# Performance work log

Measured on AMD Instinct MI355X. Metric: run time of the kernel, lower is better.

## Reference

```python
import jax, jax.numpy as jnp
import numpy as np

N, T, H, D, E, P, R = 50000, 16, 512, 256, 200000, 100000, 3
LN_EPS = 1e-5
BN_EPS = 1e-5


def setup_inputs() -> dict:
    key = jax.random.key(0)
    ks = jax.random.split(key, 32)
    ri = lambda k, shape, hi: jax.random.randint(k, shape, 0, hi)
    rn = lambda k, shape, scale=0.05: (jax.random.normal(k, shape, dtype=jnp.float32) * scale)
    return {
        "node_type_ids": ri(ks[0], (N,), T),
        "src0": ri(ks[1], (E,), N), "dst0": ri(ks[2], (E,), N),
        "src1": ri(ks[3], (E,), N), "dst1": ri(ks[4], (E,), N),
        "src2": ri(ks[5], (E,), N), "dst2": ri(ks[6], (E,), N),
        "pairs": ri(ks[7], (2, P), N),
        "degrees": ri(ks[8], (N,), 100),
        "node_emb": rn(ks[9], (N, H)),
        "type_emb": rn(ks[10], (T, H)),
        "w_loop_in": rn(ks[11], (H, H)),
        "w_rel_in": rn(ks[12], (R, H, H)),
        "w_loop_res": rn(ks[13], (H, H)),
        "w_rel_res": rn(ks[14], (R, H, H)),
        "ln_g": jnp.ones((H,), jnp.float32),
        "ln_b": jnp.zeros((H,), jnp.float32),
        "w_loop_out": rn(ks[15], (H, D)),
        "w_rel_out": rn(ks[16], (R, H, D)),
        "lp_w1": rn(ks[17], (3 * D, D)),
        "lp_b1": jnp.zeros((D,), jnp.float32),
        "bn_g": jnp.ones((D,), jnp.float32),
        "bn_b": jnp.zeros((D,), jnp.float32),
        "bn_mean": jnp.zeros((D,), jnp.float32),
        "bn_var": jnp.ones((D,), jnp.float32),
        "lp_w2": rn(ks[18], (D, 1)),
        "lp_b2": jnp.zeros((1,), jnp.float32),
        "alpha": jnp.float32(0.1),
        "beta": jnp.float32(0.1),
    }


def _rgcn(x, loop_w, rel_w, srcs, dsts):
    # out = x @ W_loop + sum_r (A_r @ x) @ W_r ; A_r unweighted COO -> segment_sum
    out = x @ loop_w
    for r in range(R):
        msg = jax.ops.segment_sum(x[srcs[r]], dsts[r], num_segments=x.shape[0])
        out = out + msg @ rel_w[r]
    return out


def _layernorm(h, g, b):
    mu = h.mean(-1, keepdims=True)
    var = h.var(-1, keepdims=True)
    return (h - mu) * jax.lax.rsqrt(var + LN_EPS) * g + b


def reference(node_type_ids, src0, dst0, src1, dst1, src2, dst2, pairs, degrees,
              node_emb, type_emb, w_loop_in, w_rel_in, w_loop_res, w_rel_res,
              ln_g, ln_b, w_loop_out, w_rel_out, lp_w1, lp_b1, bn_g, bn_b,
              bn_mean, bn_var, lp_w2, lp_b2, alpha, beta):
    srcs = (src0, src1, src2)
    dsts = (dst0, dst1, dst2)
    # encode
    x = node_emb + type_emb[node_type_ids]          # [N, H]
    x = jax.nn.relu(_rgcn(x, w_loop_in, w_rel_in, srcs, dsts))
    h = _rgcn(x, w_loop_res, w_rel_res, srcs, dsts)
    h = jax.nn.relu(_layernorm(h, ln_g, ln_b))      # dropout p=0 -> identity
    x = x + h
    z = _rgcn(x, w_loop_out, w_rel_out, srcs, dsts)  # [N, D]
    # score
    src_z = z[pairs[0]]                              # [P, D]
    dst_z = z[pairs[1]]
    src_deg = jnp.clip(degrees[pairs[0]], 1).astype(jnp.float32)
    dst_deg = jnp.clip(degrees[pairs[1]], 1).astype(jnp.float32)
    feats = jnp.concatenate([src_z, dst_z, src_z * dst_z], axis=-1)  # [P, 3D]
    h1 = jax.nn.relu(feats @ lp_w1 + lp_b1)
    # BatchNorm1d in eval mode: running stats
    h1 = (h1 - bn_mean) * jax.lax.rsqrt(bn_var + BN_EPS) * bn_g + bn_b
    mlp_score = (h1 @ lp_w2 + lp_b2).squeeze(-1)     # [P]
    base = mlp_score - jax.nn.relu(alpha) * jnp.log(src_deg) - jax.nn.relu(beta) * jnp.log(dst_deg)
    return base / (jnp.sqrt(src_deg) * jnp.sqrt(dst_deg) + 1e-8)
```

## Files before the change

### kernel.cpp

```cpp
#include <hip/hip_runtime.h>

typedef __attribute__((ext_vector_type(8))) _Float16 half8;
typedef __attribute__((ext_vector_type(4))) _Float16 half4;
typedef __attribute__((ext_vector_type(4))) float f32x4;

static __device__ __forceinline__ void gload16(const void* g, void* l) {
  __builtin_amdgcn_global_load_lds((const __attribute__((address_space(1))) void*)g,
                                   (__attribute__((address_space(3))) void*)l, 16, 0, 0);
}

__global__ void k_encode(const float* __restrict__ emb, const float* __restrict__ temb,
                         const int* __restrict__ tids, _Float16* __restrict__ x, int n) {
  int i = blockIdx.x * 256 + threadIdx.x;
  if (i >= n * 64) return;
  int node = i >> 6, c = (i & 63) << 3;
  const float* e = emb + (size_t)node * 512 + c;
  const float* t = temb + (size_t)tids[node] * 512 + c;
  float4 a0 = *(const float4*)e, a1 = *(const float4*)(e + 4);
  float4 b0 = *(const float4*)t, b1 = *(const float4*)(t + 4);
  half8 o;
  o[0] = (_Float16)(a0.x + b0.x); o[1] = (_Float16)(a0.y + b0.y);
  o[2] = (_Float16)(a0.z + b0.z); o[3] = (_Float16)(a0.w + b0.w);
  o[4] = (_Float16)(a1.x + b1.x); o[5] = (_Float16)(a1.y + b1.y);
  o[6] = (_Float16)(a1.z + b1.z); o[7] = (_Float16)(a1.w + b1.w);
  *(half8*)(x + (size_t)node * 512 + c) = o;
}

__global__ void k_zero(int* __restrict__ p, int n) {
  int i = blockIdx.x * 256 + threadIdx.x;
  if (i < n) p[i] = 0;
}

__global__ void k_hist(const int* __restrict__ d0, const int* __restrict__ d1,
                       const int* __restrict__ d2, int* __restrict__ counts, int E, int Np1) {
  int e = blockIdx.x * 256 + threadIdx.x;
  if (e >= E) return;
  int r = blockIdx.y;
  const int* d = (r == 0) ? d0 : ((r == 1) ? d1 : d2);
  atomicAdd(&counts[r * Np1 + d[e] + 1], 1);
}

__global__ void k_scan(const int* __restrict__ counts, int* __restrict__ rowp, int n) {
  __shared__ int wsum[16];
  int r = blockIdx.x;
  const int* c = counts + (size_t)r * n;
  int* o = rowp + (size_t)r * n;
  int lane = threadIdx.x & 63, w = threadIdx.x >> 6;
  int off = 0;
  for (int base = 0; base < n; base += 1024) {
    int i = base + threadIdx.x;
    int v = (i < n) ? c[i] : 0;
    int sc = v;
    #pragma unroll
    for (int d = 1; d < 64; d <<= 1) {
      int t = __shfl_up(sc, (unsigned)d);
      if (lane >= d) sc += t;
    }
    if (lane == 63) wsum[w] = sc;
    __syncthreads();
    int wo = 0, tot = 0;
    #pragma unroll
    for (int ww = 0; ww < 16; ++ww) {
      int s = wsum[ww];
      if (ww < w) wo += s;
      tot += s;
    }
    if (i < n) o[i] = sc + wo + off;
    off += tot;
    __syncthreads();
  }
}

__global__ void k_copy(const int* __restrict__ a, int* __restrict__ b, int n) {
  int i = blockIdx.x * 256 + threadIdx.x;
  if (i < n) b[i] = a[i];
}

__global__ void k_fill(const int* __restrict__ s0, const int* __restrict__ s1, const int* __restrict__ s2,
                       const int* __restrict__ d0, const int* __restrict__ d1, const int* __restrict__ d2,
                       int* __restrict__ cursor, int* __restrict__ col_src, int E, int Np1) {
  int e = blockIdx.x * 256 + threadIdx.x;
  if (e >= E) return;
  int r = blockIdx.y;
  const int* dp = (r == 0) ? d0 : ((r == 1) ? d1 : d2);
  const int* sp = (r == 0) ? s0 : ((r == 1) ? s1 : s2);
  int pos = atomicAdd(&cursor[r * Np1 + dp[e]], 1);
  if (pos >= 0 && pos < E) col_src[(size_t)r * E + pos] = sp[e];
}

__global__ void k_aggregate(const _Float16* __restrict__ x, _Float16* __restrict__ agg,
                            const int* __restrict__ rowp, const int* __restrict__ col_src,
                            int N, int E) {
  int wid = (blockIdx.x * 256 + threadIdx.x) >> 6;
  int lane = threadIdx.x & 63;
  if (wid >= 3 * N) return;
  int r = wid / N;
  int n = wid - r * N;
  int beg = rowp[r * (N + 1) + n], end = rowp[r * (N + 1) + n + 1];
  const int* cs = col_src + (size_t)r * E;
  float acc[8] = {0, 0, 0, 0, 0, 0, 0, 0};
  for (int e = beg; e < end; ++e) {
    int s = cs[e];
    half8 v = *(const half8*)(x + (size_t)s * 512 + lane * 8);
    #pragma unroll
    for (int j = 0; j < 8; ++j) acc[j] += (float)v[j];
  }
  half8 o;
  #pragma unroll
  for (int j = 0; j < 8; ++j) o[j] = (_Float16)acc[j];
  *(half8*)(agg + (size_t)n * 1536 + r * 512 + lane * 8) = o;
}

__global__ void k_transpose(const float* __restrict__ Bl, const float* __restrict__ Br,
                            _Float16* __restrict__ Bt, int No, int K) {
  __shared__ float tile[64][65];
  int k0 = blockIdx.x * 64, n0 = blockIdx.y * 64;
  int nl = threadIdx.x & 63, kb = threadIdx.x >> 6;
  #pragma unroll
  for (int i = 0; i < 16; ++i) {
    int kl = kb + i * 4;
    int krow = k0 + kl;
    float v = (krow < 512) ? Bl[(size_t)krow * No + n0 + nl]
                           : Br[(size_t)(krow - 512) * No + n0 + nl];
    tile[kl][nl] = v;
  }
  __syncthreads();
  int kl = threadIdx.x & 63, nb = threadIdx.x >> 6;
  #pragma unroll
  for (int i = 0; i < 16; ++i) {
    int n2 = nb + i * 4;
    Bt[(size_t)(n0 + n2) * K + k0 + kl] = (_Float16)tile[kl][n2];
  }
}

__global__ __launch_bounds__(256) void k_gemm_rgcn(
    const _Float16* __restrict__ Ain, const _Float16* __restrict__ Aagg,
    const _Float16* __restrict__ Bt, _Float16* __restrict__ C,
    int M, int Ncols, int K, int relu) {
  __shared__ __align__(16) _Float16 As[128 * 32];
  __shared__ __align__(16) _Float16 Bs[128 * 32];
  int tid = threadIdx.x;
  int bn0 = blockIdx.x * 128, bm0 = blockIdx.y * 128;
  int lane = tid & 63, wv = tid >> 6;
  int wm = wv & 1, wn = wv >> 1;
  int l16 = lane & 15, quad = lane >> 4;

  int rl = wv * 16 + (lane >> 2);
  int kq = (lane & 3) * 8;
  int ra0 = bm0 + rl;       if (ra0 >= M) ra0 = M - 1;
  int ra1 = bm0 + 64 + rl;  if (ra1 >= M) ra1 = M - 1;
  int rb0 = bn0 + rl, rb1 = bn0 + 64 + rl;

  const _Float16* pa0 = Ain + (size_t)ra0 * 512 + kq;
  const _Float16* pa1 = Ain + (size_t)ra1 * 512 + kq;
  const _Float16* pb0 = Bt + (size_t)rb0 * K + kq;
  const _Float16* pb1 = Bt + (size_t)rb1 * K + kq;
  _Float16* la0 = &As[(wv * 16) * 32];
  _Float16* la1 = &As[(64 + wv * 16) * 32];
  _Float16* lb0 = &Bs[(wv * 16) * 32];
  _Float16* lb1 = &Bs[(64 + wv * 16) * 32];

  f32x4 acc[4][4];
  #pragma unroll
  for (int i = 0; i < 4; ++i)
    #pragma unroll
    for (int j = 0; j < 4; ++j) acc[i][j] = (f32x4){0.f, 0.f, 0.f, 0.f};

  for (int k0 = 0; k0 < K; k0 += 32) {
    if (k0 == 512) {
      pa0 = Aagg + (size_t)ra0 * 1536 + kq;
      pa1 = Aagg + (size_t)ra1 * 1536 + kq;
    }
    __syncthreads();
    gload16(pa0, la0);
    gload16(pa1, la1);
    gload16(pb0, lb0);
    gload16(pb1, lb1);
    __syncthreads();
    half8 af[4], bf[4];
    #pragma unroll
    for (int i = 0; i < 4; ++i)
      af[i] = *(const half8*)&As[(wm * 64 + i * 16 + l16) * 32 + quad * 8];
    #pragma unroll
    for (int j = 0; j < 4; ++j)
      bf[j] = *(const half8*)&Bs[(wn * 64 + j * 16 + l16) * 32 + quad * 8];
    #pragma unroll
    for (int i = 0; i < 4; ++i)
      #pragma unroll
      for (int j = 0; j < 4; ++j)
        acc[i][j] = __builtin_amdgcn_mfma_f32_16x16x32_f16(af[i], bf[j], acc[i][j], 0, 0, 0);
    pa0 += 32; pa1 += 32; pb0 += 32; pb1 += 32;
  }

  #pragma unroll
  for (int i = 0; i < 4; ++i)
    #pragma unroll
    for (int j = 0; j < 4; ++j)
      #pragma unroll
      for (int rg = 0; rg < 4; ++rg) {
        int row = bm0 + wm * 64 + i * 16 + quad * 4 + rg;
        int col = bn0 + wn * 64 + j * 16 + l16;
        if (row < M) {
          float v = acc[i][j][rg];
          if (relu) v = fmaxf(v, 0.f);
          C[(size_t)row * Ncols + col] = (_Float16)v;
        }
      }
}

#define LSTR 40

__global__ __launch_bounds__(256) void k_gemm_link(
    const _Float16* __restrict__ z, const int* __restrict__ pairs,
    const _Float16* __restrict__ Bt,
    const float* __restrict__ b1, const float* __restrict__ bng, const float* __restrict__ bnb,
    const float* __restrict__ bnm, const float* __restrict__ bnv,
    _Float16* __restrict__ h1, int P, int K) {
  __shared__ __align__(16) _Float16 As[128 * LSTR];
  __shared__ __align__(16) _Float16 Bs[128 * LSTR];
  int tid = threadIdx.x;
  int bn0 = blockIdx.x * 128, bm0 = blockIdx.y * 128;
  int lane = tid & 63, wv = tid >> 6;
  int wm = wv & 1, wn = wv >> 1;
  int l16 = lane & 15, quad = lane >> 4;
  int srow = tid >> 1, scs = (tid & 1) * 16;
  int p = bm0 + srow; if (p >= P) p = P - 1;
  int sp = pairs[p], dp = pairs[P + p];
  const _Float16* zs = z + (size_t)sp * 256;
  const _Float16* zd = z + (size_t)dp * 256;
  int bgn = bn0 + srow;

  f32x4 acc[4][4];
  #pragma unroll
  for (int i = 0; i < 4; ++i)
    #pragma unroll
    for (int j = 0; j < 4; ++j) acc[i][j] = (f32x4){0.f, 0.f, 0.f, 0.f};

  for (int k0 = 0; k0 < K; k0 += 32) {
    __syncthreads();
    int seg = k0 >> 8;
    int kk = (k0 & 255) + scs;
    __attribute__((aligned(16))) _Float16 tmp[16];
    if (seg == 0) {
      *(uint4*)tmp = *(const uint4*)(zs + kk);
      *(uint4*)(tmp + 8) = *(const uint4*)(zs + kk + 8);
    } else if (seg == 1) {
      *(uint4*)tmp = *(const uint4*)(zd + kk);
      *(uint4*)(tmp + 8) = *(const uint4*)(zd + kk + 8);
    } else {
      half8 u0 = *(const half8*)(zs + kk), u1 = *(const half8*)(zs + kk + 8);
      half8 v0 = *(const half8*)(zd + kk), v1 = *(const half8*)(zd + kk + 8);
      #pragma unroll
      for (int j = 0; j < 8; ++j) {
        tmp[j] = (_Float16)((float)u0[j] * (float)v0[j]);
        tmp[j + 8] = (_Float16)((float)u1[j] * (float)v1[j]);
      }
    }
    *(uint4*)&As[srow * LSTR + scs] = *(const uint4*)tmp;
    *(uint4*)&As[srow * LSTR + scs + 8] = *(const uint4*)(tmp + 8);
    {
      const _Float16* src = Bt + (size_t)bgn * K + k0 + scs;
      *(uint4*)&Bs[srow * LSTR + scs] = *(const uint4*)src;
      *(uint4*)&Bs[srow * LSTR + scs + 8] = *(const uint4*)(src + 8);
    }
    __syncthreads();
    half8 af[4], bf[4];
    #pragma unroll
    for (int i = 0; i < 4; ++i)
      af[i] = *(const half8*)&As[(wm * 64 + i * 16 + l16) * LSTR + quad * 8];
    #pragma unroll
    for (int j = 0; j < 4; ++j)
      bf[j] = *(const half8*)&Bs[(wn * 64 + j * 16 + l16) * LSTR + quad * 8];
    #pragma unroll
    for (int i = 0; i < 4; ++i)
      #pragma unroll
      for (int j = 0; j < 4; ++j)
        acc[i][j] = __builtin_amdgcn_mfma_f32_16x16x32_f16(af[i], bf[j], acc[i][j], 0, 0, 0);
  }

  #pragma unroll
  for (int i = 0; i < 4; ++i)
    #pragma unroll
    for (int j = 0; j < 4; ++j) {
      int col = bn0 + wn * 64 + j * 16 + l16;
      float bb1 = b1[col], m = bnm[col], rs = rsqrtf(bnv[col] + 1e-5f);
      float gg = bng[col], bb = bnb[col];
      #pragma unroll
      for (int rg = 0; rg < 4; ++rg) {
        int row = bm0 + wm * 64 + i * 16 + quad * 4 + rg;
        if (row < P) {
          float v = fmaxf(acc[i][j][rg] + bb1, 0.f);
          v = (v - m) * rs * gg + bb;
          h1[(size_t)row * 256 + col] = (_Float16)v;
        }
      }
    }
}

__global__ void k_ln_res(const _Float16* __restrict__ h, const _Float16* __restrict__ x1,
                         const float* __restrict__ g, const float* __restrict__ b,
                         _Float16* __restrict__ out, int N) {
  int wid = (blockIdx.x * 256 + threadIdx.x) >> 6;
  int lane = threadIdx.x & 63;
  if (wid >= N) return;
  int c = lane * 8;
  half8 hv = *(const half8*)(h + (size_t)wid * 512 + c);
  float hf[8];
  float s = 0.f, sq = 0.f;
  #pragma unroll
  for (int j = 0; j < 8; ++j) {
    hf[j] = (float)hv[j];
    s += hf[j];
    sq += hf[j] * hf[j];
  }
  #pragma unroll
  for (int off = 32; off; off >>= 1) {
    s += __shfl_down(s, (unsigned)off);
    sq += __shfl_down(sq, (unsigned)off);
  }
  s = __shfl(s, 0); sq = __shfl(sq, 0);
  float mu = s * (1.f / 512.f);
  float var = sq * (1.f / 512.f) - mu * mu;
  float rs = rsqrtf(var + 1e-5f);
  float4 g0 = *(const float4*)(g + c), g1 = *(const float4*)(g + c + 4);
  float4 b0 = *(const float4*)(b + c), b1 = *(const float4*)(b + c + 4);
  float gf[8] = {g0.x, g0.y, g0.z, g0.w, g1.x, g1.y, g1.z, g1.w};
  float bf[8] = {b0.x, b0.y, b0.z, b0.w, b1.x, b1.y, b1.z, b1.w};
  half8 xv = *(const half8*)(x1 + (size_t)wid * 512 + c);
  half8 o;
  #pragma unroll
  for (int j = 0; j < 8; ++j) {
    float xw = (float)xv[j];
    o[j] = (_Float16)(xw + fmaxf((hf[j] - mu) * rs * gf[j] + bf[j], 0.f));
  }
  *(half8*)(out + (size_t)wid * 512 + c) = o;
}

__global__ void k_score(const _Float16* __restrict__ h1, const float* __restrict__ w2,
                        const float* __restrict__ b2, const int* __restrict__ pairs,
                        const int* __restrict__ degrees, const float* __restrict__ alpha,
                        const float* __restrict__ beta, float* __restrict__ out, int P) {
  int wid = (blockIdx.x * 256 + threadIdx.x) >> 6;
  int lane = threadIdx.x & 63;
  if (wid >= P) return;
  int c = lane * 4;
  half4 hv = *(const half4*)(h1 + (size_t)wid * 256 + c);
  float4 wv = *(const float4*)(w2 + c);
  float s = (float)hv[0] * wv.x + (float)hv[1] * wv.y + (float)hv[2] * wv.z + (float)hv[3] * wv.w;
  #pragma unroll
  for (int off = 32; off; off >>= 1) s += __shfl_down(s, (unsigned)off);
  if (lane == 0) {
    int sp = pairs[wid], dp = pairs[P + wid];
    float sd = (float)max(degrees[sp], 1);
    float dd = (float)max(degrees[dp], 1);
    float base = s + b2[0] - fmaxf(alpha[0], 0.f) * logf(sd) - fmaxf(beta[0], 0.f) * logf(dd);
    out[wid] = base / (sqrtf(sd) * sqrtf(dd) + 1e-8f);
  }
}

extern "C" void kernel_launch(void* const* d_in, const int* in_sizes, int n_in,
                              void* d_out, int out_size, void* d_ws, size_t ws_size,
                              hipStream_t stream) {
  const int N = 50000, E = 200000, P = 100000;
  const int Np1 = N + 1;
  const int* node_type = (const int*)d_in[0];
  const int* src0 = (const int*)d_in[1]; const int* dst0 = (const int*)d_in[2];
  const int* src1 = (const int*)d_in[3]; const int* dst1 = (const int*)d_in[4];
  const int* src2 = (const int*)d_in[5]; const int* dst2 = (const int*)d_in[6];
  const int* pairs = (const int*)d_in[7];
  const int* degrees = (const int*)d_in[8];
  const float* node_emb = (const float*)d_in[9];
  const float* type_emb = (const float*)d_in[10];
  const float* w_loop_in = (const float*)d_in[11];
  const float* w_rel_in = (const float*)d_in[12];
  const float* w_loop_res = (const float*)d_in[13];
  const float* w_rel_res = (const float*)d_in[14];
  const float* ln_g = (const float*)d_in[15];
  const float* ln_b = (const float*)d_in[16];
  const float* w_loop_out = (const float*)d_in[17];
  const float* w_rel_out = (const float*)d_in[18];
  const float* lp_w1 = (const float*)d_in[19];
  const float* lp_b1 = (const float*)d_in[20];
  const float* bn_g = (const float*)d_in[21];
  const float* bn_b = (const float*)d_in[22];
  const float* bn_mean = (const float*)d_in[23];
  const float* bn_var = (const float*)d_in[24];
  const float* lp_w2 = (const float*)d_in[25];
  const float* lp_b2 = (const float*)d_in[26];
  const float* alpha = (const float*)d_in[27];
  const float* beta = (const float*)d_in[28];
  float* out = (float*)d_out;

  char* ws = (char*)d_ws;
  size_t off = 0;
  auto alloc = [&](size_t bytes) {
    void* p = ws + off;
    off = (off + bytes + 255) & ~(size_t)255;
    return p;
  };
  _Float16* xb0 = (_Float16*)alloc((size_t)N * 512 * 2);
  _Float16* xb1 = (_Float16*)alloc((size_t)N * 512 * 2);
  _Float16* agg = (_Float16*)alloc((size_t)N * 1536 * 2);
  _Float16* Bt = (_Float16*)alloc((size_t)512 * 2048 * 2);
  int* counts = (int*)alloc((size_t)3 * Np1 * 4);
  int* rowp = (int*)alloc((size_t)3 * Np1 * 4);
  int* cursor = (int*)alloc((size_t)3 * Np1 * 4);
  int* col_src = (int*)alloc((size_t)3 * E * 4);
  if (off > ws_size) return;

  _Float16* z = xb1;
  _Float16* h1 = agg;

  k_zero<<<(3 * Np1 + 255) / 256, 256, 0, stream>>>(counts, 3 * Np1);
  dim3 gE((E + 255) / 256, 3);
  k_hist<<<gE, 256, 0, stream>>>(dst0, dst1, dst2, counts, E, Np1);
  k_scan<<<3, 1024, 0, stream>>>(counts, rowp, Np1);
  k_copy<<<(3 * Np1 + 255) / 256, 256, 0, stream>>>(rowp, cursor, 3 * Np1);
  k_fill<<<gE, 256, 0, stream>>>(src0, src1, src2, dst0, dst1, dst2, cursor, col_src, E, Np1);

  k_encode<<<(N * 64 + 255) / 256, 256, 0, stream>>>(node_emb, type_emb, node_type, xb0, N);

  int aggBlocks = (3 * N + 3) / 4;
  dim3 g1(4, (N + 127) / 128);
  dim3 g3(2, (N + 127) / 128);

  k_aggregate<<<aggBlocks, 256, 0, stream>>>(xb0, agg, rowp, col_src, N, E);
  k_transpose<<<dim3(32, 8), 256, 0, stream>>>(w_loop_in, w_rel_in, Bt, 512, 2048);
  k_gemm_rgcn<<<g1, 256, 0, stream>>>(xb0, agg, Bt, xb1, N, 512, 2048, 1);

  k_aggregate<<<aggBlocks, 256, 0, stream>>>(xb1, agg, rowp, col_src, N, E);
  k_transpose<<<dim3(32, 8), 256, 0, stream>>>(w_loop_res, w_rel_res, Bt, 512, 2048);
  k_gemm_rgcn<<<g1, 256, 0, stream>>>(xb1, agg, Bt, xb0, N, 512, 2048, 0);

  k_ln_res<<<(N + 3) / 4, 256, 0, stream>>>(xb0, xb1, ln_g, ln_b, xb0, N);

  k_aggregate<<<aggBlocks, 256, 0, stream>>>(xb0, agg, rowp, col_src, N, E);
  k_transpose<<<dim3(32, 4), 256, 0, stream>>>(w_loop_out, w_rel_out, Bt, 256, 2048);
  k_gemm_rgcn<<<g3, 256, 0, stream>>>(xb0, agg, Bt, z, N, 256, 2048, 0);

  k_transpose<<<dim3(12, 4), 256, 0, stream>>>(lp_w1, lp_w1 + 512 * 256, Bt, 256, 768);
  dim3 gl(2, (P + 127) / 128);
  k_gemm_link<<<gl, 256, 0, stream>>>(z, pairs, Bt, lp_b1, bn_g, bn_b, bn_mean, bn_var, h1, P, 768);

  k_score<<<(P + 3) / 4, 256, 0, stream>>>(h1, lp_w2, lp_b2, pairs, degrees, alpha, beta, out, P);
}
```

Measured before the change: 1.263 ms.

## Widen GEMM K-tile to 64 with XOR-swizzled LDS and grouped block order

The RGCN GEMM now stages 64-wide K slices instead of 32, halving the number of barrier pairs per K sweep. LDS rows are XOR-swizzled so the global-to-LDS loads and the fragment reads avoid bank conflicts. Blocks are launched on a 1D grid remapped into groups of 8 row tiles that sweep all column tiles, to improve L2 reuse of the A rows. This doubles LDS use per block, which may reduce occupancy.

```diff
diff --git a/kernel.cpp b/kernel.cpp
--- a/kernel.cpp
+++ b/kernel.cpp
@@ -136,29 +136,41 @@
 __global__ __launch_bounds__(256) void k_gemm_rgcn(
     const _Float16* __restrict__ Ain, const _Float16* __restrict__ Aagg,
     const _Float16* __restrict__ Bt, _Float16* __restrict__ C,
-    int M, int Ncols, int K, int relu) {
-  __shared__ __align__(16) _Float16 As[128 * 32];
-  __shared__ __align__(16) _Float16 Bs[128 * 32];
+    int M, int Ncols, int K, int relu, int S, int T) {
+  __shared__ __align__(16) _Float16 As[128 * 64];
+  __shared__ __align__(16) _Float16 Bs[128 * 64];
+  int lin = blockIdx.x;
+  int grp = lin / (8 * T);
+  int rmd = lin - grp * 8 * T;
+  int c = rmd >> 3, x = rmd & 7;
+  int s = grp * 8 + x;
+  if (s >= S) return;
+  int bm0 = s * 128, bn0 = c * 128;
+
   int tid = threadIdx.x;
-  int bn0 = blockIdx.x * 128, bm0 = blockIdx.y * 128;
   int lane = tid & 63, wv = tid >> 6;
   int wm = wv & 1, wn = wv >> 1;
   int l16 = lane & 15, quad = lane >> 4;
 
-  int rl = wv * 16 + (lane >> 2);
-  int kq = (lane & 3) * 8;
-  int ra0 = bm0 + rl;       if (ra0 >= M) ra0 = M - 1;
-  int ra1 = bm0 + 64 + rl;  if (ra1 >= M) ra1 = M - 1;
-  int rb0 = bn0 + rl, rb1 = bn0 + 64 + rl;
-
-  const _Float16* pa0 = Ain + (size_t)ra0 * 512 + kq;
-  const _Float16* pa1 = Ain + (size_t)ra1 * 512 + kq;
-  const _Float16* pb0 = Bt + (size_t)rb0 * K + kq;
-  const _Float16* pb1 = Bt + (size_t)rb1 * K + kq;
-  _Float16* la0 = &As[(wv * 16) * 32];
-  _Float16* la1 = &As[(64 + wv * 16) * 32];
-  _Float16* lb0 = &Bs[(wv * 16) * 32];
-  _Float16* lb1 = &Bs[(64 + wv * 16) * 32];
+  int rl8 = lane >> 3;
+  int gs = (lane & 7) ^ rl8;
+  int rA[4], rB[4];
+  const _Float16* pa[4];
+  const _Float16* pb[4];
+  _Float16* ldA[4];
+  _Float16* ldB[4];
+  #pragma unroll
+  for (int q = 0; q < 4; ++q) {
+    int chunk = wv * 4 + q;
+    int rl = chunk * 8 + rl8;
+    int ra = bm0 + rl; if (ra >= M) ra = M - 1;
+    rA[q] = ra;
+    rB[q] = bn0 + rl;
+    pa[q] = Ain + (size_t)ra * 512 + gs * 8;
+    pb[q] = Bt + (size_t)rB[q] * K + gs * 8;
+    ldA[q] = &As[chunk * 8 * 64];
+    ldB[q] = &Bs[chunk * 8 * 64];
+  }
 
   f32x4 acc[4][4];
   #pragma unroll
@@ -166,30 +178,35 @@
     #pragma unroll
     for (int j = 0; j < 4; ++j) acc[i][j] = (f32x4){0.f, 0.f, 0.f, 0.f};
 
-  for (int k0 = 0; k0 < K; k0 += 32) {
+  for (int k0 = 0; k0 < K; k0 += 64) {
     if (k0 == 512) {
-      pa0 = Aagg + (size_t)ra0 * 1536 + kq;
-      pa1 = Aagg + (size_t)ra1 * 1536 + kq;
-    }
-    __syncthreads();
-    gload16(pa0, la0);
-    gload16(pa1, la1);
-    gload16(pb0, lb0);
-    gload16(pb1, lb1);
-    __syncthreads();
-    half8 af[4], bf[4];
-    #pragma unroll
-    for (int i = 0; i < 4; ++i)
-      af[i] = *(const half8*)&As[(wm * 64 + i * 16 + l16) * 32 + quad * 8];
-    #pragma unroll
-    for (int j = 0; j < 4; ++j)
-      bf[j] = *(const half8*)&Bs[(wn * 64 + j * 16 + l16) * 32 + quad * 8];
-    #pragma unroll
-    for (int i = 0; i < 4; ++i)
+      #pragma unroll
+      for (int q = 0; q < 4; ++q) pa[q] = Aagg + (size_t)rA[q] * 1536 + gs * 8;
+    }
+    __syncthreads();
+    #pragma unroll
+    for (int q = 0; q < 4; ++q) gload16(pa[q], ldA[q]);
+    #pragma unroll
+    for (int q = 0; q < 4; ++q) gload16(pb[q], ldB[q]);
+    __syncthreads();
+    #pragma unroll
+    for (int sb = 0; sb < 2; ++sb) {
+      half8 af[4], bf[4];
+      int slot = ((sb * 4 + quad) ^ (l16 & 7)) * 8;
+      #pragma unroll
+      for (int i = 0; i < 4; ++i)
+        af[i] = *(const half8*)&As[(wm * 64 + i * 16 + l16) * 64 + slot];
       #pragma unroll
       for (int j = 0; j < 4; ++j)
-        acc[i][j] = __builtin_amdgcn_mfma_f32_16x16x32_f16(af[i], bf[j], acc[i][j], 0, 0, 0);
-    pa0 += 32; pa1 += 32; pb0 += 32; pb1 += 32;
+        bf[j] = *(const half8*)&Bs[(wn * 64 + j * 16 + l16) * 64 + slot];
+      #pragma unroll
+      for (int i = 0; i < 4; ++i)
+        #pragma unroll
+        for (int j = 0; j < 4; ++j)
+          acc[i][j] = __builtin_amdgcn_mfma_f32_16x16x32_f16(af[i], bf[j], acc[i][j], 0, 0, 0);
+    }
+    #pragma unroll
+    for (int q = 0; q < 4; ++q) { pa[q] += 64; pb[q] += 64; }
   }
 
   #pragma unroll
@@ -421,22 +438,23 @@
   k_encode<<<(N * 64 + 255) / 256, 256, 0, stream>>>(node_emb, type_emb, node_type, xb0, N);
 
   int aggBlocks = (3 * N + 3) / 4;
-  dim3 g1(4, (N + 127) / 128);
-  dim3 g3(2, (N + 127) / 128);
+  const int S = (N + 127) / 128;
+  int blocks4 = ((S + 7) / 8) * 8 * 4;
+  int blocks2 = ((S + 7) / 8) * 8 * 2;
 
   k_aggregate<<<aggBlocks, 256, 0, stream>>>(xb0, agg, rowp, col_src, N, E);
   k_transpose<<<dim3(32, 8), 256, 0, stream>>>(w_loop_in, w_rel_in, Bt, 512, 2048);
-  k_gemm_rgcn<<<g1, 256, 0, stream>>>(xb0, agg, Bt, xb1, N, 512, 2048, 1);
+  k_gemm_rgcn<<<blocks4, 256, 0, stream>>>(xb0, agg, Bt, xb1, N, 512, 2048, 1, S, 4);
 
   k_aggregate<<<aggBlocks, 256, 0, stream>>>(xb1, agg, rowp, col_src, N, E);
   k_transpose<<<dim3(32, 8), 256, 0, stream>>>(w_loop_res, w_rel_res, Bt, 512, 2048);
-  k_gemm_rgcn<<<g1, 256, 0, stream>>>(xb1, agg, Bt, xb0, N, 512, 2048, 0);
+  k_gemm_rgcn<<<blocks4, 256, 0, stream>>>(xb1, agg, Bt, xb0, N, 512, 2048, 0, S, 4);
 
   k_ln_res<<<(N + 3) / 4, 256, 0, stream>>>(xb0, xb1, ln_g, ln_b, xb0, N);
 
   k_aggregate<<<aggBlocks, 256, 0, stream>>>(xb0, agg, rowp, col_src, N, E);
   k_transpose<<<dim3(32, 4), 256, 0, stream>>>(w_loop_out, w_rel_out, Bt, 256, 2048);
-  k_gemm_rgcn<<<g3, 256, 0, stream>>>(xb0, agg, Bt, z, N, 256, 2048, 0);
+  k_gemm_rgcn<<<blocks2, 256, 0, stream>>>(xb0, agg, Bt, z, N, 256, 2048, 0, S, 2);
 
   k_transpose<<<dim3(12, 4), 256, 0, stream>>>(lp_w1, lp_w1 + 512 * 256, Bt, 256, 768);
   dim3 gl(2, (P + 127) / 128);
```

Measured after the change: 1.134 ms. 1.11x faster.
